# Kernel optimization log

Measured on AMD Instinct MI355X. Metric: run time of the kernel, lower is better.

## Reference

```python
import jax, jax.numpy as jnp
import numpy as np

NUM_HEADS = 12
DIM = 768
HEAD_DIM = DIM // NUM_HEADS


def setup_inputs() -> dict:
    key = jax.random.key(0)
    ks = jax.random.split(key, 10)
    B, S = 4, 2048
    x = jax.random.normal(ks[0], (B, S, DIM), dtype=jnp.float32)
    attn_mask = jnp.zeros((B, S), dtype=jnp.float32)  # additive mask
    scale = 0.02
    Wq = jax.random.normal(ks[1], (DIM, DIM), dtype=jnp.float32) * scale
    bq = jnp.zeros((DIM,), dtype=jnp.float32)
    Wk = jax.random.normal(ks[2], (DIM, DIM), dtype=jnp.float32) * scale
    bk = jnp.zeros((DIM,), dtype=jnp.float32)
    Wv = jax.random.normal(ks[3], (DIM, DIM), dtype=jnp.float32) * scale
    bv = jnp.zeros((DIM,), dtype=jnp.float32)
    Wo = jax.random.normal(ks[4], (DIM, DIM), dtype=jnp.float32) * scale
    bo = jnp.zeros((DIM,), dtype=jnp.float32)
    return {"x": x, "attn_mask": attn_mask, "Wq": Wq, "bq": bq,
            "Wk": Wk, "bk": bk, "Wv": Wv, "bv": bv, "Wo": Wo, "bo": bo}


def reference(x, attn_mask, Wq, bq, Wk, bk, Wv, bv, Wo, bo):
    B, S, D = x.shape
    H, Hd = NUM_HEADS, HEAD_DIM
    scaling = Hd ** -0.5

    def split_heads(e):  # [B,S,D] -> [B,H,S,Hd]
        return e.reshape(B, S, H, Hd).transpose(0, 2, 1, 3)

    q = split_heads((x @ Wq + bq) * scaling)
    k = split_heads(x @ Wk + bk)
    v = split_heads(x @ Wv + bv)

    scores = jnp.einsum('bhqd,bhkd->bhqk', q, k)
    scores = scores + attn_mask[:, None, None, :]  # additive mask [B,1,1,S]
    probs = jax.nn.softmax(scores, axis=-1)
    out = jnp.einsum('bhqk,bhkd->bhqd', probs, v)  # [B,H,S,Hd]
    out = out.transpose(0, 2, 1, 3).reshape(B, S, D)
    return out @ Wo + bo
```

## Files before the change

### kernel.cpp

```cpp
#include <hip/hip_runtime.h>
#include <hip/hip_bf16.h>
#include <cstdint>
#include <cstddef>

#define DIM   768
#define NH    12
#define HD    64
#define BATCH 4
#define SEQ   2048
#define MTOT  (BATCH*SEQ)
#define NQKV  (3*DIM)

#define LOG2E 1.4426950408889634f

typedef __attribute__((ext_vector_type(8))) short bf16x8;
typedef __attribute__((ext_vector_type(4))) short bf16x4;
typedef __attribute__((ext_vector_type(4))) float f32x4;

__device__ __forceinline__ short f2bf(float f){
  union { __hip_bfloat16 h; short s; } u;
  u.h = __float2bfloat16(f);
  return u.s;
}

#if defined(__HIP_DEVICE_COMPILE__) && __has_builtin(__builtin_amdgcn_exp2f)
#define EXP2(x) __builtin_amdgcn_exp2f(x)
#else
#define EXP2(x) exp2f(x)
#endif

__device__ __forceinline__ f32x4 mfma32(bf16x8 a, bf16x8 b, f32x4 c){
  return __builtin_amdgcn_mfma_f32_16x16x32_bf16(a, b, c, 0, 0, 0);
}

__device__ __forceinline__ void gl_lds16(const short* g, short* l){
  __builtin_amdgcn_global_load_lds(
      (const __attribute__((address_space(1))) unsigned int*)g,
      (__attribute__((address_space(3))) unsigned int*)l,
      16, 0, 0);
}

#define VMCNT(N) asm volatile("s_waitcnt vmcnt(" #N ")" ::: "memory")
#define BARRIER() __builtin_amdgcn_s_barrier()

__device__ __forceinline__ size_t img_idx(int m, int k){
  const int mt = m >> 7, r = m & 127, ks = k >> 5, c = k & 31;
  return ((size_t)(mt*24 + ks))*4096 + (size_t)((r>>6)*2048 + ((r>>4)&3)*512
       + ((r&15) + ((c>>3)<<4))*8 + (c&7));
}


__global__ __launch_bounds__(256) void pack_all(
    const float* __restrict__ x,
    const float* __restrict__ Wq, const float* __restrict__ Wk,
    const float* __restrict__ Wv, const float* __restrict__ Wo,
    const float* __restrict__ bq, const float* __restrict__ bk,
    const float* __restrict__ bv, const float* __restrict__ mask,
    short* __restrict__ xb, short* __restrict__ wqkv, short* __restrict__ wot,
    float* __restrict__ bqkv, float* __restrict__ mask2)
{
  const int NX4 = MTOT*DIM/4;
  const int NW4 = DIM*DIM/4;
  int gid = blockIdx.x * 256 + threadIdx.x;

  if (gid < NX4){
    float4 v = ((const float4*)x)[gid];
    const int e = gid*4;
    const int m = e / DIM, k = e - m*DIM;
    bf16x4 o;
    o[0] = f2bf(v.x); o[1] = f2bf(v.y); o[2] = f2bf(v.z); o[3] = f2bf(v.w);
    *(bf16x4*)&xb[img_idx(m, k)] = o;
    return;
  }
  gid -= NX4;
  if (gid < 4*NW4){
    const int mat = gid / NW4;
    const int rem = gid - mat*NW4;
    const int e = rem*4;
    const int k = e / DIM, n = e - k*DIM;
    const float* W = (mat == 0) ? Wq : (mat == 1) ? Wk : (mat == 2) ? Wv : Wo;
    const float4 v = *(const float4*)&W[e];
    short* img = (mat < 3) ? wqkv : wot;
    const int ng = (mat < 3) ? mat*DIM + n : n;
    img[img_idx(ng+0, k)] = f2bf(v.x);
    img[img_idx(ng+1, k)] = f2bf(v.y);
    img[img_idx(ng+2, k)] = f2bf(v.z);
    img[img_idx(ng+3, k)] = f2bf(v.w);
    return;
  }
  gid -= 4*NW4;
  if (gid < NQKV)
    bqkv[gid] = (gid < DIM) ? bq[gid] : (gid < 2*DIM) ? bk[gid-DIM] : bv[gid-2*DIM];
  if (gid < BATCH*SEQ)
    mask2[gid] = mask[gid] * LOG2E;
}


template<int MODE>
__global__ __launch_bounds__(256, 3) void gemm_lds(
    const short* __restrict__ Aimg,
    const short* __restrict__ Bimg,
    const float* __restrict__ bias,
    short* __restrict__ o0, short* __restrict__ o1, short* __restrict__ o2,
    float* __restrict__ fo)
{
  __shared__ short ldsA[3*4096];
  __shared__ short ldsB[3*4096];

  const int tid = threadIdx.x;
  const int w  = tid >> 6, l = tid & 63;
  const int lr = l & 15,  lg = l >> 4;
  const int wr = w >> 1,  wc = w & 1;
  const int mt = blockIdx.x, nt = blockIdx.y;
  const int mBase = mt * 128;
  const int nBase = nt * 128;

  const short* gA = Aimg + (size_t)mt*24*4096 + w*512 + l*8;
  const short* gB = Bimg + (size_t)nt*24*4096 + w*512 + l*8;

#define STAGE(BUF, KS) do {                                                \
    gl_lds16(gA + (KS)*4096,        &ldsA[(BUF)*4096 + w*512]);            \
    gl_lds16(gA + (KS)*4096 + 2048, &ldsA[(BUF)*4096 + 2048 + w*512]);     \
    gl_lds16(gB + (KS)*4096,        &ldsB[(BUF)*4096 + w*512]);            \
    gl_lds16(gB + (KS)*4096 + 2048, &ldsB[(BUF)*4096 + 2048 + w*512]);     \
  } while(0)

#define GCOMP(CUR) do {                                                    \
    bf16x8 a[4], b[4];                                                     \
    _Pragma("unroll")                                                      \
    for (int i = 0; i < 4; ++i){                                           \
      a[i] = *(const bf16x8*)&ldsA[(CUR)*4096 + wr*2048 + i*512 + l*8];    \
      b[i] = *(const bf16x8*)&ldsB[(CUR)*4096 + wc*2048 + i*512 + l*8];    \
    }                                                                      \
    _Pragma("unroll")                                                      \
    for (int i = 0; i < 4; ++i)                                            \
      _Pragma("unroll")                                                    \
      for (int j = 0; j < 4; ++j)                                          \
        acc[i][j] = mfma32(a[i], b[j], acc[i][j]);                         \
  } while(0)

  f32x4 acc[4][4] = {};
  STAGE(0, 0);
  STAGE(1, 1);
  int cur = 0;
  for (int kt = 0; kt < 23; ++kt){
    VMCNT(4);
    BARRIER();
    if (kt < 22){
      int nb = cur + 2; if (nb >= 3) nb -= 3;
      STAGE(nb, kt+2);
    }
    GCOMP(cur);
    cur = (cur == 2) ? 0 : cur + 1;
  }
  VMCNT(0);
  BARRIER();
  GCOMP(cur);
#undef STAGE
#undef GCOMP

  if (MODE == 0){
    const int sect  = nBase / DIM;
    const int nloc0 = nBase - sect*DIM + wc*64;
    const float scl = (sect == 0) ? 0.125f*LOG2E : 1.0f;
#pragma unroll
    for (int j = 0; j < 4; ++j){
      const int nl = nloc0 + j*16 + lr;
      const int h = nl >> 6, d = nl & (HD-1);
      const float bn = bias[nBase + wc*64 + j*16 + lr];
#pragma unroll
      for (int i = 0; i < 4; ++i){
        const int m0 = mBase + wr*64 + i*16 + lg*4;
        const int b_ = m0 >> 11, s0 = m0 & (SEQ-1);
        const int bh = b_*NH + h;
        if (sect == 2){
          const int p0 = (((s0>>2)&3)<<3) | (((s0>>4)&1)<<2);
          const size_t idx = (((size_t)bh*64 + (s0>>5))*4 + (d>>4))*512
                           + ((d&15) + (p0>>3)*16)*8 + (p0&7);
          bf16x4 ov;
#pragma unroll
          for (int r = 0; r < 4; ++r) ov[r] = f2bf((acc[i][j][r] + bn));
          *(bf16x4*)&o2[idx] = ov;
        } else {
#pragma unroll
          for (int r = 0; r < 4; ++r){
            const int s_ = s0 + r;
            const float val = (acc[i][j][r] + bn) * scl;
            if (sect == 0){
              o0[((size_t)bh*SEQ + s_)*HD + d] = f2bf(val);
            } else {
              const size_t idx = (((size_t)bh*64 + (s_>>5))*4
                                  + ((s_>>4)&1)*2 + (d>>5))*512
                               + ((s_&15) + ((d>>3)&3)*16)*8 + (d&7);
              o1[idx] = f2bf(val);
            }
          }
        }
      }
    }
  } else {
#pragma unroll
    for (int j = 0; j < 4; ++j){
      const int n = nBase + wc*64 + j*16 + lr;
      const float bn = bias[n];
#pragma unroll
      for (int i = 0; i < 4; ++i){
#pragma unroll
        for (int r = 0; r < 4; ++r){
          const int m = mBase + wr*64 + i*16 + lg*4 + r;
          fo[(size_t)m * DIM + n] = acc[i][j][r] + bn;
        }
      }
    }
  }
}


__global__ __launch_bounds__(256, 3) void attn_kernel(
    const short* __restrict__ q,
    const short* __restrict__ kimg,
    const short* __restrict__ vimg,
    const float* __restrict__ mask2,
    short* __restrict__ ao)
{
  __shared__ short ldsK[3*4096];
  __shared__ short ldsV[3*4096];

  const int tid = threadIdx.x;
  const int l = tid & 63, w = tid >> 6;
  const int lr = l & 15, lg = l >> 4;
  const int bh = blockIdx.x;
  const int b_ = bh / NH;
  const int h  = bh - b_*NH;
  const int qbase = blockIdx.y * 128 + w * 32;

  const short* qh   = q + (size_t)bh * SEQ * HD;
  const short* kSrc = kimg + (size_t)bh * 64 * 2048 + w*512 + l*8;
  const short* vSrc = vimg + (size_t)bh * 64 * 2048 + w*512 + l*8;
  const float* mRow = mask2 + (size_t)b_ * SEQ + lg*4;

  bf16x8 qf[2][2];
#pragma unroll
  for (int t = 0; t < 2; ++t){
    qf[t][0] = *(const bf16x8*)&qh[(size_t)(qbase + t*16 + lr)*HD + lg*8];
    qf[t][1] = *(const bf16x8*)&qh[(size_t)(qbase + t*16 + lr)*HD + 32 + lg*8];
  }

  bf16x8 ones;
#pragma unroll
  for (int j = 0; j < 8; ++j) ones[j] = (short)0x3F80;

  f32x4 o[2][4] = {};
  f32x4 lacc[2] = {};

#define ASTAGE(BUF, ST) do {                                                 \
    gl_lds16(kSrc + (size_t)(ST)*4096,        &ldsK[(BUF)*4096 + w*512]);    \
    gl_lds16(kSrc + (size_t)(ST)*4096 + 2048, &ldsK[(BUF)*4096+2048+w*512]); \
    gl_lds16(vSrc + (size_t)(ST)*4096,        &ldsV[(BUF)*4096 + w*512]);    \
    gl_lds16(vSrc + (size_t)(ST)*4096 + 2048, &ldsV[(BUF)*4096+2048+w*512]); \
  } while(0)

#define ACOMP(ST, CUR) do {                                                  \
    _Pragma("unroll")                                                        \
    for (int sub = 0; sub < 2; ++sub){                                       \
      bf16x8 kf[4], vf[4];                                                   \
      _Pragma("unroll")                                                      \
      for (int f = 0; f < 4; ++f){                                           \
        kf[f] = *(const bf16x8*)&ldsK[(CUR)*4096 + sub*2048 + f*512 + l*8];  \
        vf[f] = *(const bf16x8*)&ldsV[(CUR)*4096 + sub*2048 + f*512 + l*8];  \
      }                                                                      \
      const int koff = (ST)*64 + sub*32;                                     \
      const float4 mv0 = *(const float4*)(mRow + koff);                      \
      const float4 mv1 = *(const float4*)(mRow + koff + 16);                 \
      bf16x8 pf[2];                                                          \
      _Pragma("unroll")                                                      \
      for (int t = 0; t < 2; ++t){                                           \
        f32x4 s0 = {}, s1 = {};                                              \
        s0 = mfma32(kf[0], qf[t][0], s0);                                    \
        s0 = mfma32(kf[1], qf[t][1], s0);                                    \
        s1 = mfma32(kf[2], qf[t][0], s1);                                    \
        s1 = mfma32(kf[3], qf[t][1], s1);                                    \
        const float p0 = EXP2(s0[0] + mv0.x);                                \
        const float p1 = EXP2(s0[1] + mv0.y);                                \
        const float p2 = EXP2(s0[2] + mv0.z);                                \
        const float p3 = EXP2(s0[3] + mv0.w);                                \
        const float p4 = EXP2(s1[0] + mv1.x);                                \
        const float p5 = EXP2(s1[1] + mv1.y);                                \
        const float p6 = EXP2(s1[2] + mv1.z);                                \
        const float p7 = EXP2(s1[3] + mv1.w);                                \
        pf[t][0]=f2bf(p0); pf[t][1]=f2bf(p1); pf[t][2]=f2bf(p2); pf[t][3]=f2bf(p3); \
        pf[t][4]=f2bf(p4); pf[t][5]=f2bf(p5); pf[t][6]=f2bf(p6); pf[t][7]=f2bf(p7); \
      }                                                                      \
      __builtin_amdgcn_s_setprio(1);                                         \
      _Pragma("unroll")                                                      \
      for (int dblk = 0; dblk < 4; ++dblk){                                  \
        o[0][dblk] = mfma32(vf[dblk], pf[0], o[0][dblk]);                    \
        o[1][dblk] = mfma32(vf[dblk], pf[1], o[1][dblk]);                    \
      }                                                                      \
      lacc[0] = mfma32(ones, pf[0], lacc[0]);                                \
      lacc[1] = mfma32(ones, pf[1], lacc[1]);                                \
      __builtin_amdgcn_s_setprio(0);                                         \
    }                                                                        \
  } while(0)

  ASTAGE(0, 0);
  ASTAGE(1, 1);
  int cur = 0;
  for (int st = 0; st < 31; ++st){
    if (st == 0)      VMCNT(4);
    else if (st == 1) VMCNT(8);
    else              VMCNT(12);
    BARRIER();
    if (st < 30){
      int nb = cur + 2; if (nb >= 3) nb -= 3;
      ASTAGE(nb, st+2);
    }
    ACOMP(st, cur);
    cur = (cur == 2) ? 0 : cur + 1;
  }
  VMCNT(8);
  BARRIER();
  ACOMP(31, cur);
#undef ASTAGE
#undef ACOMP

#pragma unroll
  for (int t = 0; t < 2; ++t){
    const float rinv = 1.f / lacc[t][0];
    const int m = b_*SEQ + qbase + t*16 + lr;
    const int mt = m >> 7, r = m & 127;
    short* abase = ao + (size_t)mt*24*4096
                 + (r>>6)*2048 + ((r>>4)&3)*512;
#pragma unroll
    for (int dblk = 0; dblk < 4; ++dblk){
      bf16x4 ov;
#pragma unroll
      for (int rr = 0; rr < 4; ++rr) ov[rr] = f2bf(o[t][dblk][rr] * rinv);
      const int k = h*64 + dblk*16 + lg*4;
      const int ks = k >> 5, c = k & 31;
      *(bf16x4*)&abase[(size_t)ks*4096 + ((r&15) + ((c>>3)<<4))*8 + (c&7)] = ov;
    }
  }
}


extern "C" void kernel_launch(void* const* d_in, const int* in_sizes, int n_in,
                              void* d_out, int out_size, void* d_ws, size_t ws_size,
                              hipStream_t stream) {
  const float* x    = (const float*)d_in[0];
  const float* mask = (const float*)d_in[1];
  const float* Wq   = (const float*)d_in[2];
  const float* bq   = (const float*)d_in[3];
  const float* Wk   = (const float*)d_in[4];
  const float* bk   = (const float*)d_in[5];
  const float* Wv   = (const float*)d_in[6];
  const float* bv   = (const float*)d_in[7];
  const float* Wo   = (const float*)d_in[8];
  const float* bo   = (const float*)d_in[9];
  float* out = (float*)d_out;

  char* ws = (char*)d_ws;
  const size_t SZ_XB = (size_t)MTOT * DIM * sizeof(short);
  const size_t SZ_W  = (size_t)DIM * DIM * sizeof(short);

  short* xb   = (short*)ws;            ws += SZ_XB;
  short* wqkv = (short*)ws;            ws += 3*SZ_W;
  short* wot  = (short*)ws;            ws += SZ_W;
  short* qb   = (short*)ws;            ws += SZ_XB;
  short* kimg = (short*)ws;            ws += SZ_XB;
  short* vimg = (short*)ws;            ws += SZ_XB;
  short* ao   = (short*)ws;            ws += SZ_XB;
  float* bqkv = (float*)ws;            ws += NQKV * sizeof(float);
  float* mask2= (float*)ws;            ws += (size_t)BATCH*SEQ*sizeof(float);

  const int NPACK = MTOT*DIM/4 + DIM*DIM + BATCH*SEQ;
  pack_all<<<(NPACK + 255)/256, 256, 0, stream>>>(
      x, Wq, Wk, Wv, Wo, bq, bk, bv, mask, xb, wqkv, wot, bqkv, mask2);

  dim3 qkvgrid(MTOT/128, NQKV/128);
  gemm_lds<0><<<qkvgrid, 256, 0, stream>>>(xb, wqkv, bqkv, qb, kimg, vimg, nullptr);

  dim3 agrid(BATCH*NH, SEQ/128);
  attn_kernel<<<agrid, 256, 0, stream>>>(qb, kimg, vimg, mask2, ao);

  dim3 ogrid(MTOT/128, DIM/128);
  gemm_lds<1><<<ogrid, 256, 0, stream>>>(ao, wot, bo, nullptr, nullptr, nullptr, out);
}
```

Measured before the change: 148.1 us.

## Split key dimension across wave pairs in attention with LDS reduction

```diff
diff --git a/kernel.cpp b/kernel.cpp
--- a/kernel.cpp
+++ b/kernel.cpp
@@ -223,35 +223,34 @@
     const float* __restrict__ mask2,
     short* __restrict__ ao)
 {
-  __shared__ short ldsK[3*4096];
-  __shared__ short ldsV[3*4096];
+  __shared__ short ldsbuf[2][3*4096];
 
   const int tid = threadIdx.x;
   const int l = tid & 63, w = tid >> 6;
   const int lr = l & 15, lg = l >> 4;
+  const int pair = w >> 1, half = w & 1;
   const int bh = blockIdx.x;
   const int b_ = bh / NH;
   const int h  = bh - b_*NH;
-  const int qbase = blockIdx.y * 128 + w * 32;
+  const int qbase = blockIdx.y * 128 + pair * 64;
+
+  short* ldsK = &ldsbuf[0][0];
+  short* ldsV = &ldsbuf[1][0];
 
   const short* qh   = q + (size_t)bh * SEQ * HD;
   const short* kSrc = kimg + (size_t)bh * 64 * 2048 + w*512 + l*8;
   const short* vSrc = vimg + (size_t)bh * 64 * 2048 + w*512 + l*8;
   const float* mRow = mask2 + (size_t)b_ * SEQ + lg*4;
 
-  bf16x8 qf[2][2];
-#pragma unroll
-  for (int t = 0; t < 2; ++t){
+  bf16x8 qf[4][2];
+#pragma unroll
+  for (int t = 0; t < 4; ++t){
     qf[t][0] = *(const bf16x8*)&qh[(size_t)(qbase + t*16 + lr)*HD + lg*8];
     qf[t][1] = *(const bf16x8*)&qh[(size_t)(qbase + t*16 + lr)*HD + 32 + lg*8];
   }
 
-  bf16x8 ones;
-#pragma unroll
-  for (int j = 0; j < 8; ++j) ones[j] = (short)0x3F80;
-
-  f32x4 o[2][4] = {};
-  f32x4 lacc[2] = {};
+  f32x4 o[4][4] = {};
+  float lsum[4] = {0.f, 0.f, 0.f, 0.f};
 
 #define ASTAGE(BUF, ST) do {                                                 \
     gl_lds16(kSrc + (size_t)(ST)*4096,        &ldsK[(BUF)*4096 + w*512]);    \
@@ -261,44 +260,40 @@
   } while(0)
 
 #define ACOMP(ST, CUR) do {                                                  \
+    bf16x8 kf[4], vf[4];                                                     \
     _Pragma("unroll")                                                        \
-    for (int sub = 0; sub < 2; ++sub){                                       \
-      bf16x8 kf[4], vf[4];                                                   \
-      _Pragma("unroll")                                                      \
-      for (int f = 0; f < 4; ++f){                                           \
-        kf[f] = *(const bf16x8*)&ldsK[(CUR)*4096 + sub*2048 + f*512 + l*8];  \
-        vf[f] = *(const bf16x8*)&ldsV[(CUR)*4096 + sub*2048 + f*512 + l*8];  \
-      }                                                                      \
-      const int koff = (ST)*64 + sub*32;                                     \
-      const float4 mv0 = *(const float4*)(mRow + koff);                      \
-      const float4 mv1 = *(const float4*)(mRow + koff + 16);                 \
-      bf16x8 pf[2];                                                          \
-      _Pragma("unroll")                                                      \
-      for (int t = 0; t < 2; ++t){                                           \
-        f32x4 s0 = {}, s1 = {};                                              \
-        s0 = mfma32(kf[0], qf[t][0], s0);                                    \
-        s0 = mfma32(kf[1], qf[t][1], s0);                                    \
-        s1 = mfma32(kf[2], qf[t][0], s1);                                    \
-        s1 = mfma32(kf[3], qf[t][1], s1);                                    \
-        const float p0 = EXP2(s0[0] + mv0.x);                                \
-        const float p1 = EXP2(s0[1] + mv0.y);                                \
-        const float p2 = EXP2(s0[2] + mv0.z);                                \
-        const float p3 = EXP2(s0[3] + mv0.w);                                \
-        const float p4 = EXP2(s1[0] + mv1.x);                                \
-        const float p5 = EXP2(s1[1] + mv1.y);                                \
-        const float p6 = EXP2(s1[2] + mv1.z);                                \
-        const float p7 = EXP2(s1[3] + mv1.w);                                \
-        pf[t][0]=f2bf(p0); pf[t][1]=f2bf(p1); pf[t][2]=f2bf(p2); pf[t][3]=f2bf(p3); \
-        pf[t][4]=f2bf(p4); pf[t][5]=f2bf(p5); pf[t][6]=f2bf(p6); pf[t][7]=f2bf(p7); \
-      }                                                                      \
+    for (int f = 0; f < 4; ++f){                                             \
+      kf[f] = *(const bf16x8*)&ldsK[(CUR)*4096 + half*2048 + f*512 + l*8];   \
+      vf[f] = *(const bf16x8*)&ldsV[(CUR)*4096 + half*2048 + f*512 + l*8];   \
+    }                                                                        \
+    const int koff = (ST)*64 + half*32;                                      \
+    const float4 mv0 = *(const float4*)(mRow + koff);                        \
+    const float4 mv1 = *(const float4*)(mRow + koff + 16);                   \
+    _Pragma("unroll")                                                        \
+    for (int t = 0; t < 4; ++t){                                             \
+      f32x4 s0 = {mv0.x, mv0.y, mv0.z, mv0.w};                               \
+      f32x4 s1 = {mv1.x, mv1.y, mv1.z, mv1.w};                               \
+      s0 = mfma32(kf[0], qf[t][0], s0);                                      \
+      s0 = mfma32(kf[1], qf[t][1], s0);                                      \
+      s1 = mfma32(kf[2], qf[t][0], s1);                                      \
+      s1 = mfma32(kf[3], qf[t][1], s1);                                      \
+      const float p0 = EXP2(s0[0]);                                          \
+      const float p1 = EXP2(s0[1]);                                          \
+      const float p2 = EXP2(s0[2]);                                          \
+      const float p3 = EXP2(s0[3]);                                          \
+      const float p4 = EXP2(s1[0]);                                          \
+      const float p5 = EXP2(s1[1]);                                          \
+      const float p6 = EXP2(s1[2]);                                          \
+      const float p7 = EXP2(s1[3]);                                          \
+      lsum[t] += ((p0+p1)+(p2+p3)) + ((p4+p5)+(p6+p7));                      \
+      bf16x8 pf;                                                             \
+      pf[0]=f2bf(p0); pf[1]=f2bf(p1); pf[2]=f2bf(p2); pf[3]=f2bf(p3);        \
+      pf[4]=f2bf(p4); pf[5]=f2bf(p5); pf[6]=f2bf(p6); pf[7]=f2bf(p7);        \
       __builtin_amdgcn_s_setprio(1);                                         \
-      _Pragma("unroll")                                                      \
-      for (int dblk = 0; dblk < 4; ++dblk){                                  \
-        o[0][dblk] = mfma32(vf[dblk], pf[0], o[0][dblk]);                    \
-        o[1][dblk] = mfma32(vf[dblk], pf[1], o[1][dblk]);                    \
-      }                                                                      \
-      lacc[0] = mfma32(ones, pf[0], lacc[0]);                                \
-      lacc[1] = mfma32(ones, pf[1], lacc[1]);                                \
+      o[t][0] = mfma32(vf[0], pf, o[t][0]);                                  \
+      o[t][1] = mfma32(vf[1], pf, o[t][1]);                                  \
+      o[t][2] = mfma32(vf[2], pf, o[t][2]);                                  \
+      o[t][3] = mfma32(vf[3], pf, o[t][3]);                                  \
       __builtin_amdgcn_s_setprio(0);                                         \
     }                                                                        \
   } while(0)
@@ -308,8 +303,8 @@
   int cur = 0;
   for (int st = 0; st < 31; ++st){
     if (st == 0)      VMCNT(4);
-    else if (st == 1) VMCNT(8);
-    else              VMCNT(12);
+    else if (st == 1) VMCNT(6);
+    else              VMCNT(8);
     BARRIER();
     if (st < 30){
       int nb = cur + 2; if (nb >= 3) nb -= 3;
@@ -318,27 +313,51 @@
     ACOMP(st, cur);
     cur = (cur == 2) ? 0 : cur + 1;
   }
-  VMCNT(8);
+  VMCNT(2);
   BARRIER();
   ACOMP(31, cur);
 #undef ASTAGE
 #undef ACOMP
 
 #pragma unroll
-  for (int t = 0; t < 2; ++t){
-    const float rinv = 1.f / lacc[t][0];
-    const int m = b_*SEQ + qbase + t*16 + lr;
-    const int mt = m >> 7, r = m & 127;
-    short* abase = ao + (size_t)mt*24*4096
-                 + (r>>6)*2048 + ((r>>4)&3)*512;
-#pragma unroll
-    for (int dblk = 0; dblk < 4; ++dblk){
-      bf16x4 ov;
-#pragma unroll
-      for (int rr = 0; rr < 4; ++rr) ov[rr] = f2bf(o[t][dblk][rr] * rinv);
-      const int k = h*64 + dblk*16 + lg*4;
-      const int ks = k >> 5, c = k & 31;
-      *(bf16x4*)&abase[(size_t)ks*4096 + ((r&15) + ((c>>3)<<4))*8 + (c&7)] = ov;
+  for (int t = 0; t < 4; ++t){
+    lsum[t] += __shfl_xor(lsum[t], 16);
+    lsum[t] += __shfl_xor(lsum[t], 32);
+  }
+
+  __syncthreads();
+  float* red  = (float*)&ldsbuf[0][0];
+  float* redl = ((float*)&ldsbuf[0][0]) + 8192;
+  if (half == 1){
+#pragma unroll
+    for (int t = 0; t < 4; ++t){
+#pragma unroll
+      for (int dblk = 0; dblk < 4; ++dblk)
+        *(f32x4*)&red[pair*4096 + t*1024 + dblk*256 + l*4] = o[t][dblk];
+      if (lg == 0) redl[pair*64 + t*16 + lr] = lsum[t];
+    }
+  }
+  __syncthreads();
+  if (half == 0){
+#pragma unroll
+    for (int t = 0; t < 4; ++t){
+      const float ltot = lsum[t] + redl[pair*64 + t*16 + lr];
+      const float rinv = 1.f / ltot;
+      const int m = b_*SEQ + qbase + t*16 + lr;
+      const int mt = m >> 7, r = m & 127;
+      short* abase = ao + (size_t)mt*24*4096
+                   + (r>>6)*2048 + ((r>>4)&3)*512;
+#pragma unroll
+      for (int dblk = 0; dblk < 4; ++dblk){
+        const f32x4 op = *(const f32x4*)&red[pair*4096 + t*1024 + dblk*256 + l*4];
+        bf16x4 ov;
+#pragma unroll
+        for (int rr = 0; rr < 4; ++rr)
+          ov[rr] = f2bf((o[t][dblk][rr] + op[rr]) * rinv);
+        const int k = h*64 + dblk*16 + lg*4;
+        const int ks = k >> 5, c = k & 31;
+        *(bf16x4*)&abase[(size_t)ks*4096 + ((r&15) + ((c>>3)<<4))*8 + (c&7)] = ov;
+      }
     }
   }
 }
```

Result: slower. 158.8 us (+7.2%).
